# Kernel tuning notes

Measured on AMD Instinct MI355X. Metric: run time of the kernel, lower is better.

The kernel has to match this reference:

```python
import jax, jax.numpy as jnp
import numpy as np

F_IN = 22 * 1000   # flattened EEG trial
D_DENSE = 100      # Dense(100) -> becomes T=100 timesteps of dim 1
H = 128            # LSTM units
N_CLASS = 4


def setup_inputs() -> dict:
    key = jax.random.key(0)
    ks = jax.random.split(key, 8)
    B = 4096
    s1 = 1.0 / np.sqrt(F_IN)
    sr = 1.0 / np.sqrt(H)
    x = jax.random.normal(ks[0], (B, 22, 1000), dtype=jnp.float32)
    W1 = jax.random.uniform(ks[1], (F_IN, D_DENSE), jnp.float32, -s1, s1)
    b1 = jnp.zeros((D_DENSE,), jnp.float32)
    # Keras LSTM kernels: input kernel [1, 4H], recurrent kernel [H, 4H], bias [4H]
    Wk = jax.random.uniform(ks[2], (1, 4 * H), jnp.float32, -1.0, 1.0)
    Wr = jax.random.normal(ks[3], (H, 4 * H), dtype=jnp.float32) * sr
    # Keras unit_forget_bias: f-gate bias initialized to 1
    bl = jnp.concatenate([jnp.zeros(H), jnp.ones(H), jnp.zeros(2 * H)]).astype(jnp.float32)
    W2 = jax.random.uniform(ks[4], (H, N_CLASS), jnp.float32, -sr, sr)
    b2 = jnp.zeros((N_CLASS,), jnp.float32)
    return {"x": x, "W1": W1, "b1": b1, "Wk": Wk, "Wr": Wr, "bl": bl, "W2": W2, "b2": b2}


def _lstm_last(seq, Wk, Wr, bl):
    # seq: [B, T, 1]; returns final hidden state [B, H]
    B = seq.shape[0]
    # precompute input contribution for all steps: [T, B, 4H]
    zx = jnp.einsum('btf,fg->tbg', seq, Wk) + bl

    def step(carry, zxt):
        h, c = carry
        z = zxt + h @ Wr                      # [B, 4H]
        i, f, g, o = jnp.split(z, 4, axis=-1)  # keras gate order: i, f, c, o
        i = jax.nn.sigmoid(i)
        f = jax.nn.sigmoid(f)
        g = jnp.tanh(g)
        o = jax.nn.sigmoid(o)
        c = f * c + i * g
        h = o * jnp.tanh(c)
        return (h, c), None

    init = (jnp.zeros((B, H), seq.dtype), jnp.zeros((B, H), seq.dtype))
    (h, _), _ = jax.lax.scan(step, init, zx)
    return h


def reference(x, W1, b1, Wk, Wr, bl, W2, b2):
    B = x.shape[0]
    flat = x.reshape(B, -1)                 # Flatten
    d = flat @ W1 + b1                      # Dense(100), linear activation
    seq = d.reshape(B, D_DENSE, 1)          # Reshape((100, 1))
    h = _lstm_last(seq, Wk, Wr, bl)         # LSTM(128) -> last hidden state
    logits = h @ W2 + b2                    # Dense(4)
    return jax.nn.softmax(logits, axis=-1)
```

## Files before the change

kernel.cpp:

```cpp
#include <hip/hip_runtime.h>
#include <stdint.h>

#define F_IN   22000
#define B_SZ   4096
#define T_STEPS 100
#define NSPLIT 16
#define NCHUNK 22
#define KSPAN  (NCHUNK * 64)
#define ACC_STRIDE 104
#define ACCB_BYTES ((size_t)B_SZ * ACC_STRIDE * 4)
#define BIMG_BYTES 28672
#define BIMG_HALF  14336
#define W1IMG_BYTES ((size_t)NSPLIT * NCHUNK * BIMG_BYTES)

typedef float f32x4 __attribute__((ext_vector_type(4)));
typedef short s16x8 __attribute__((ext_vector_type(8)));

__device__ inline unsigned short f2bf(float f){
  unsigned u = __builtin_bit_cast(unsigned, f);
  u += 0x7FFFu + ((u >> 16) & 1u);
  return (unsigned short)(u >> 16);
}
__device__ inline float bf2f(unsigned short h){
  return __builtin_bit_cast(float, ((unsigned)h) << 16);
}
__device__ inline float sigf(float x){
  return __builtin_amdgcn_rcpf(1.f + __expf(-x));
}
__device__ inline float tanhf_(float x){
  return 1.f - 2.f * __builtin_amdgcn_rcpf(__expf(2.f * x) + 1.f);
}

__global__ __launch_bounds__(256) void k_zero(float4* __restrict__ p, int n4){
  int i = blockIdx.x * 256 + threadIdx.x;
  if (i < n4) p[i] = make_float4(0.f, 0.f, 0.f, 0.f);
}

__global__ __launch_bounds__(256) void k_w1img(const float* __restrict__ W1,
                                               char* __restrict__ img){
  int ch = blockIdx.x, s = blockIdx.y;
  int k0 = s * KSPAN + ch * 64;
  char* base = img + ((size_t)(s * NCHUNK + ch)) * BIMG_BYTES;
  int tid = threadIdx.x;
  #pragma unroll
  for (int it = 0; it < 4; ++it){
    int task = it * 256 + tid;
    if (task < 896){
      int p  = task * 16;
      int c  = p >> 7;
      int k8 = ((p >> 4) & 7) ^ (c & 7);
      unsigned hw[4], lw[4];
      #pragma unroll
      for (int jj = 0; jj < 4; ++jj){
        float v0 = 0.f, v1 = 0.f;
        int k = k0 + k8 * 8 + jj * 2;
        if (c < 100){
          if (k     < F_IN) v0 = W1[(size_t)k * 100 + c];
          if (k + 1 < F_IN) v1 = W1[(size_t)(k + 1) * 100 + c];
        }
        unsigned short h0 = f2bf(v0), l0 = f2bf(v0 - bf2f(h0));
        unsigned short h1 = f2bf(v1), l1 = f2bf(v1 - bf2f(h1));
        hw[jj] = (unsigned)h0 | ((unsigned)h1 << 16);
        lw[jj] = (unsigned)l0 | ((unsigned)l1 << 16);
      }
      *(uint4*)(base + p)             = make_uint4(hw[0], hw[1], hw[2], hw[3]);
      *(uint4*)(base + BIMG_HALF + p) = make_uint4(lw[0], lw[1], lw[2], lw[3]);
    }
  }
}

__global__ __launch_bounds__(256, 4) void k_dense(const float* __restrict__ x,
                                                  const float* __restrict__ W1,
                                                  const char* __restrict__ img,
                                                  float* __restrict__ accb,
                                                  int use_img){
  __shared__ char Bimg[BIMG_BYTES];
  int tid = threadIdx.x;
  int lane = tid & 63, w = tid >> 6;
  int r = lane & 15, oct = lane >> 4;
  int brow = blockIdx.x * 64;
  int s = blockIdx.y;
  int arow = brow + w * 16 + r;
  const float* xrow = x + (size_t)arow * F_IN;

  f32x4 acc[7];
  #pragma unroll
  for (int i = 0; i < 7; ++i) acc[i] = (f32x4)0.f;

  for (int ch = 0; ch < NCHUNK; ++ch){
    int k0 = s * KSPAN + ch * 64;
    int ka0 = k0 + oct * 8;
    int ka1 = k0 + 32 + oct * 8;
    float4 a0 = make_float4(0,0,0,0), a1 = a0, a2 = a0, a3 = a0;
    if (ka0 < F_IN){ a0 = *(const float4*)(xrow + ka0); a1 = *(const float4*)(xrow + ka0 + 4); }
    if (ka1 < F_IN){ a2 = *(const float4*)(xrow + ka1); a3 = *(const float4*)(xrow + ka1 + 4); }

    __syncthreads();
    if (use_img){
      const char* src = img + ((size_t)(s * NCHUNK + ch)) * BIMG_BYTES;
      #pragma unroll
      for (int i = 0; i < 7; ++i){
        int seg = i * 4 + w;
        __builtin_amdgcn_global_load_lds(
            (const __attribute__((address_space(1))) void*)(src + seg * 1024 + lane * 16),
            (__attribute__((address_space(3))) void*)(Bimg + seg * 1024), 16, 0, 0);
      }
    } else {
      #pragma unroll
      for (int it = 0; it < 4; ++it){
        int task = it * 256 + tid;
        if (task < 896){
          int p  = task * 16;
          int c  = p >> 7;
          int k8 = ((p >> 4) & 7) ^ (c & 7);
          unsigned hw[4], lw[4];
          #pragma unroll
          for (int jj = 0; jj < 4; ++jj){
            float v0 = 0.f, v1 = 0.f;
            int k = k0 + k8 * 8 + jj * 2;
            if (c < 100){
              if (k     < F_IN) v0 = W1[(size_t)k * 100 + c];
              if (k + 1 < F_IN) v1 = W1[(size_t)(k + 1) * 100 + c];
            }
            unsigned short h0 = f2bf(v0), l0 = f2bf(v0 - bf2f(h0));
            unsigned short h1 = f2bf(v1), l1 = f2bf(v1 - bf2f(h1));
            hw[jj] = (unsigned)h0 | ((unsigned)h1 << 16);
            lw[jj] = (unsigned)l0 | ((unsigned)l1 << 16);
          }
          *(uint4*)(Bimg + p)             = make_uint4(hw[0], hw[1], hw[2], hw[3]);
          *(uint4*)(Bimg + BIMG_HALF + p) = make_uint4(lw[0], lw[1], lw[2], lw[3]);
        }
      }
    }

    s16x8 ah0, al0, ah1, al1;
    {
      float va[16] = {a0.x,a0.y,a0.z,a0.w, a1.x,a1.y,a1.z,a1.w,
                      a2.x,a2.y,a2.z,a2.w, a3.x,a3.y,a3.z,a3.w};
      #pragma unroll
      for (int j = 0; j < 8; ++j){
        unsigned short h = f2bf(va[j]);
        ah0[j] = (short)h; al0[j] = (short)f2bf(va[j] - bf2f(h));
      }
      #pragma unroll
      for (int j = 0; j < 8; ++j){
        unsigned short h = f2bf(va[8 + j]);
        ah1[j] = (short)h; al1[j] = (short)f2bf(va[8 + j] - bf2f(h));
      }
    }
    __syncthreads();

    #pragma unroll
    for (int ct = 0; ct < 7; ++ct){
      int c = ct * 16 + r;
      int byte0 = ((c * 128 + (0 * 4 + oct) * 16) ^ ((c & 7) << 4));
      int byte1 = ((c * 128 + (1 * 4 + oct) * 16) ^ ((c & 7) << 4));
      s16x8 bh0 = *(s16x8*)(Bimg + byte0);
      s16x8 bl0 = *(s16x8*)(Bimg + BIMG_HALF + byte0);
      s16x8 bh1 = *(s16x8*)(Bimg + byte1);
      s16x8 bl1 = *(s16x8*)(Bimg + BIMG_HALF + byte1);
      acc[ct] = __builtin_amdgcn_mfma_f32_16x16x32_bf16(ah0, bh0, acc[ct], 0, 0, 0);
      acc[ct] = __builtin_amdgcn_mfma_f32_16x16x32_bf16(ah0, bl0, acc[ct], 0, 0, 0);
      acc[ct] = __builtin_amdgcn_mfma_f32_16x16x32_bf16(al0, bh0, acc[ct], 0, 0, 0);
      acc[ct] = __builtin_amdgcn_mfma_f32_16x16x32_bf16(ah1, bh1, acc[ct], 0, 0, 0);
      acc[ct] = __builtin_amdgcn_mfma_f32_16x16x32_bf16(ah1, bl1, acc[ct], 0, 0, 0);
      acc[ct] = __builtin_amdgcn_mfma_f32_16x16x32_bf16(al1, bh1, acc[ct], 0, 0, 0);
    }
  }

  #pragma unroll
  for (int ct = 0; ct < 7; ++ct){
    int col = ct * 16 + r;
    if (col < 100){
      #pragma unroll
      for (int reg = 0; reg < 4; ++reg){
        int orow = brow + w * 16 + oct * 4 + reg;
        atomicAdd(&accb[(size_t)orow * ACC_STRIDE + col], acc[ct][reg]);
      }
    }
  }
}

__global__ __launch_bounds__(256, 1) void k_lstm(const float* __restrict__ accb,
                                                 const float* __restrict__ b1,
                                                 const float* __restrict__ Wk,
                                                 const float* __restrict__ Wr,
                                                 const float* __restrict__ bl,
                                                 const float* __restrict__ W2,
                                                 const float* __restrict__ b2,
                                                 float* __restrict__ out){
  __shared__ unsigned short hbuf[2][16 * 128];
  __shared__ float dld[16][ACC_STRIDE];
  __shared__ float hf[16][132];
  int tid = threadIdx.x;
  int lane = tid & 63, w = tid >> 6;
  int oct = lane >> 4, lr = lane & 15;
  int brow = blockIdx.x * 16;

  for (int i = tid; i < 2048; i += 256) hbuf[0][i] = 0;
  for (int i = tid; i < 16 * T_STEPS; i += 256){
    int r = i / T_STEPS, t = i % T_STEPS;
    dld[r][t] = accb[(size_t)(brow + r) * ACC_STRIDE + t] + b1[t];
  }

  float wkv[4][2], blv[4][2];
  s16x8 bfrag[4][2][4];
  #pragma unroll
  for (int G = 0; G < 4; ++G){
    #pragma unroll
    for (int tt = 0; tt < 2; ++tt){
      int col = G * 128 + w * 32 + tt * 16 + lr;
      wkv[G][tt] = Wk[col];
      blv[G][tt] = bl[col];
      #pragma unroll
      for (int kk = 0; kk < 4; ++kk){
        s16x8 f;
        #pragma unroll
        for (int j = 0; j < 8; ++j){
          int k = kk * 32 + oct * 8 + j;
          f[j] = (short)f2bf(Wr[(size_t)k * 512 + col]);
        }
        bfrag[G][tt][kk] = f;
      }
    }
  }
  float cst[2][4];
  #pragma unroll
  for (int tt = 0; tt < 2; ++tt)
    #pragma unroll
    for (int reg = 0; reg < 4; ++reg) cst[tt][reg] = 0.f;
  __syncthreads();

  for (int t = 0; t < T_STEPS; ++t){
    int cur = t & 1;
    f32x4 acc[4][2];
    float dv[4];
    #pragma unroll
    for (int reg = 0; reg < 4; ++reg) dv[reg] = dld[oct * 4 + reg][t];
    #pragma unroll
    for (int G = 0; G < 4; ++G)
      #pragma unroll
      for (int tt = 0; tt < 2; ++tt)
        #pragma unroll
        for (int reg = 0; reg < 4; ++reg)
          acc[G][tt][reg] = dv[reg] * wkv[G][tt] + blv[G][tt];
    #pragma unroll
    for (int kk = 0; kk < 4; ++kk){
      int abyte = (lr * 256 + kk * 64 + oct * 16) ^ ((lr & 7) << 4);
      s16x8 a = *(s16x8*)((char*)hbuf[cur] + abyte);
      #pragma unroll
      for (int G = 0; G < 4; ++G)
        #pragma unroll
        for (int tt = 0; tt < 2; ++tt)
          acc[G][tt] = __builtin_amdgcn_mfma_f32_16x16x32_bf16(a, bfrag[G][tt][kk], acc[G][tt], 0, 0, 0);
    }
    #pragma unroll
    for (int tt = 0; tt < 2; ++tt){
      #pragma unroll
      for (int reg = 0; reg < 4; ++reg){
        float iv = sigf(acc[0][tt][reg]);
        float fv = sigf(acc[1][tt][reg]);
        float gv = tanhf_(acc[2][tt][reg]);
        float ov = sigf(acc[3][tt][reg]);
        float cv = fv * cst[tt][reg] + iv * gv;
        cst[tt][reg] = cv;
        float hv = ov * tanhf_(cv);
        int row = oct * 4 + reg;
        int col = w * 32 + tt * 16 + lr;
        int byte = (row * 256 + col * 2) ^ ((row & 7) << 4);
        *(unsigned short*)((char*)hbuf[cur ^ 1] + byte) = f2bf(hv);
        if (t == T_STEPS - 1) hf[row][col] = hv;
      }
    }
    __syncthreads();
  }

  if (tid < 64){
    int row = tid >> 2, cl = tid & 3;
    float a = b2[cl];
    #pragma unroll 8
    for (int j = 0; j < 128; ++j) a += hf[row][j] * W2[j * 4 + cl];
    float m = fmaxf(a, __shfl_xor(a, 1));
    m = fmaxf(m, __shfl_xor(m, 2));
    float e = __expf(a - m);
    float se = e + __shfl_xor(e, 1);
    se += __shfl_xor(se, 2);
    out[(size_t)(brow + row) * 4 + cl] = e * __builtin_amdgcn_rcpf(se);
  }
}

extern "C" void kernel_launch(void* const* d_in, const int* in_sizes, int n_in,
                              void* d_out, int out_size, void* d_ws, size_t ws_size,
                              hipStream_t stream){
  const float* x  = (const float*)d_in[0];
  const float* W1 = (const float*)d_in[1];
  const float* b1 = (const float*)d_in[2];
  const float* Wk = (const float*)d_in[3];
  const float* Wr = (const float*)d_in[4];
  const float* bl = (const float*)d_in[5];
  const float* W2 = (const float*)d_in[6];
  const float* b2 = (const float*)d_in[7];
  float* out = (float*)d_out;

  float* accb = (float*)d_ws;
  char*  img  = (char*)d_ws + ACCB_BYTES;
  const int use_img = (ws_size >= ACCB_BYTES + W1IMG_BYTES) ? 1 : 0;
  const int n4 = B_SZ * ACC_STRIDE / 4;

  k_zero<<<(n4 + 255) / 256, 256, 0, stream>>>((float4*)accb, n4);
  if (use_img)
    k_w1img<<<dim3(NCHUNK, NSPLIT), 256, 0, stream>>>(W1, img);
  k_dense<<<dim3(B_SZ / 64, NSPLIT), 256, 0, stream>>>(x, W1, img, accb, use_img);
  k_lstm<<<B_SZ / 16, 256, 0, stream>>>(accb, b1, Wk, Wr, bl, W2, b2, out);
}
```

Baseline: 262.7 us.

## Double-buffer W1 image in LDS and prefetch next x chunk in dense GEMM

The dense kernel now uses two LDS buffers for the pre-split W1 bf16 image. The next chunk's async global-to-LDS copy and x register loads are issued before the MFMA work on the current chunk, so memory latency overlaps with compute and one barrier per chunk is removed. The fallback path that built the W1 image inside the kernel is dropped, so the workspace is assumed to be large enough. Doubling LDS use and lowering launch bounds to 2 blocks per CU reduces occupancy in exchange for the overlap.

```diff
diff --git a/kernel.cpp b/kernel.cpp
--- a/kernel.cpp
+++ b/kernel.cpp
@@ -69,12 +69,10 @@
   }
 }
 
-__global__ __launch_bounds__(256, 4) void k_dense(const float* __restrict__ x,
-                                                  const float* __restrict__ W1,
+__global__ __launch_bounds__(256, 2) void k_dense(const float* __restrict__ x,
                                                   const char* __restrict__ img,
-                                                  float* __restrict__ accb,
-                                                  int use_img){
-  __shared__ char Bimg[BIMG_BYTES];
+                                                  float* __restrict__ accb){
+  __shared__ char Bb0[BIMG_BYTES], Bb1[BIMG_BYTES];
   int tid = threadIdx.x;
   int lane = tid & 63, w = tid >> 6;
   int r = lane & 15, oct = lane >> 4;
@@ -82,91 +80,94 @@
   int s = blockIdx.y;
   int arow = brow + w * 16 + r;
   const float* xrow = x + (size_t)arow * F_IN;
+  const char* isrc = img + (size_t)s * NCHUNK * BIMG_BYTES;
+  int kbase = s * KSPAN;
 
   f32x4 acc[7];
   #pragma unroll
   for (int i = 0; i < 7; ++i) acc[i] = (f32x4)0.f;
 
-  for (int ch = 0; ch < NCHUNK; ++ch){
-    int k0 = s * KSPAN + ch * 64;
-    int ka0 = k0 + oct * 8;
-    int ka1 = k0 + 32 + oct * 8;
-    float4 a0 = make_float4(0,0,0,0), a1 = a0, a2 = a0, a3 = a0;
-    if (ka0 < F_IN){ a0 = *(const float4*)(xrow + ka0); a1 = *(const float4*)(xrow + ka0 + 4); }
-    if (ka1 < F_IN){ a2 = *(const float4*)(xrow + ka1); a3 = *(const float4*)(xrow + ka1 + 4); }
-
+  float4 xa0, xa1, xa2, xa3;
+  float4 ya0, ya1, ya2, ya3;
+
+#define ALOAD(CH, A0, A1, A2, A3) do{                                        \
+    int k0_ = kbase + (CH) * 64;                                             \
+    int ka0_ = k0_ + oct * 8;                                                \
+    int ka1_ = k0_ + 32 + oct * 8;                                           \
+    A0 = make_float4(0.f,0.f,0.f,0.f); A1 = A0; A2 = A0; A3 = A0;            \
+    if (ka0_ < F_IN){ A0 = *(const float4*)(xrow + ka0_);                    \
+                      A1 = *(const float4*)(xrow + ka0_ + 4); }              \
+    if (ka1_ < F_IN){ A2 = *(const float4*)(xrow + ka1_);                    \
+                      A3 = *(const float4*)(xrow + ka1_ + 4); }              \
+  }while(0)
+
+#define STAGE(CH, BUF) do{                                                   \
+    const char* src_ = isrc + (size_t)(CH) * BIMG_BYTES;                     \
+    _Pragma("unroll")                                                        \
+    for (int i_ = 0; i_ < 7; ++i_){                                          \
+      int seg_ = i_ * 4 + w;                                                 \
+      __builtin_amdgcn_global_load_lds(                                      \
+        (const __attribute__((address_space(1))) void*)(src_ + seg_ * 1024 + lane * 16), \
+        (__attribute__((address_space(3))) void*)((BUF) + seg_ * 1024), 16, 0, 0); \
+    }                                                                        \
+  }while(0)
+
+#define CONVMFMA(BUF, A0, A1, A2, A3) do{                                    \
+    float va_[16] = {A0.x,A0.y,A0.z,A0.w, A1.x,A1.y,A1.z,A1.w,               \
+                     A2.x,A2.y,A2.z,A2.w, A3.x,A3.y,A3.z,A3.w};              \
+    s16x8 ah0_, al0_, ah1_, al1_;                                            \
+    _Pragma("unroll")                                                        \
+    for (int j_ = 0; j_ < 8; ++j_){                                          \
+      unsigned short h_ = f2bf(va_[j_]);                                     \
+      ah0_[j_] = (short)h_; al0_[j_] = (short)f2bf(va_[j_] - bf2f(h_));      \
+    }                                                                        \
+    _Pragma("unroll")                                                        \
+    for (int j_ = 0; j_ < 8; ++j_){                                          \
+      unsigned short h_ = f2bf(va_[8 + j_]);                                 \
+      ah1_[j_] = (short)h_; al1_[j_] = (short)f2bf(va_[8 + j_] - bf2f(h_));  \
+    }                                                                        \
+    _Pragma("unroll")                                                        \
+    for (int ct_ = 0; ct_ < 7; ++ct_){                                       \
+      int c_ = ct_ * 16 + r;                                                 \
+      int byte0_ = ((c_ * 128 + oct * 16) ^ ((c_ & 7) << 4));                \
+      int byte1_ = ((c_ * 128 + 64 + oct * 16) ^ ((c_ & 7) << 4));           \
+      s16x8 bh0_ = *(s16x8*)((BUF) + byte0_);                                \
+      s16x8 bl0_ = *(s16x8*)((BUF) + BIMG_HALF + byte0_);                    \
+      s16x8 bh1_ = *(s16x8*)((BUF) + byte1_);                                \
+      s16x8 bl1_ = *(s16x8*)((BUF) + BIMG_HALF + byte1_);                    \
+      acc[ct_] = __builtin_amdgcn_mfma_f32_16x16x32_bf16(ah0_, bh0_, acc[ct_], 0, 0, 0); \
+      acc[ct_] = __builtin_amdgcn_mfma_f32_16x16x32_bf16(ah0_, bl0_, acc[ct_], 0, 0, 0); \
+      acc[ct_] = __builtin_amdgcn_mfma_f32_16x16x32_bf16(al0_, bh0_, acc[ct_], 0, 0, 0); \
+      acc[ct_] = __builtin_amdgcn_mfma_f32_16x16x32_bf16(ah1_, bh1_, acc[ct_], 0, 0, 0); \
+      acc[ct_] = __builtin_amdgcn_mfma_f32_16x16x32_bf16(ah1_, bl1_, acc[ct_], 0, 0, 0); \
+      acc[ct_] = __builtin_amdgcn_mfma_f32_16x16x32_bf16(al1_, bh1_, acc[ct_], 0, 0, 0); \
+    }                                                                        \
+  }while(0)
+
+  STAGE(0, Bb0);
+  ALOAD(0, xa0, xa1, xa2, xa3);
+  __syncthreads();
+
+  for (int ch = 0; ch < NCHUNK; ch += 2){
+    if (ch + 1 < NCHUNK){
+      STAGE(ch + 1, Bb1);
+      ALOAD(ch + 1, ya0, ya1, ya2, ya3);
+    }
+    CONVMFMA(Bb0, xa0, xa1, xa2, xa3);
     __syncthreads();
-    if (use_img){
-      const char* src = img + ((size_t)(s * NCHUNK + ch)) * BIMG_BYTES;
-      #pragma unroll
-      for (int i = 0; i < 7; ++i){
-        int seg = i * 4 + w;
-        __builtin_amdgcn_global_load_lds(
-            (const __attribute__((address_space(1))) void*)(src + seg * 1024 + lane * 16),
-            (__attribute__((address_space(3))) void*)(Bimg + seg * 1024), 16, 0, 0);
-      }
-    } else {
-      #pragma unroll
-      for (int it = 0; it < 4; ++it){
-        int task = it * 256 + tid;
-        if (task < 896){
-          int p  = task * 16;
-          int c  = p >> 7;
-          int k8 = ((p >> 4) & 7) ^ (c & 7);
-          unsigned hw[4], lw[4];
-          #pragma unroll
-          for (int jj = 0; jj < 4; ++jj){
-            float v0 = 0.f, v1 = 0.f;
-            int k = k0 + k8 * 8 + jj * 2;
-            if (c < 100){
-              if (k     < F_IN) v0 = W1[(size_t)k * 100 + c];
-              if (k + 1 < F_IN) v1 = W1[(size_t)(k + 1) * 100 + c];
-            }
-            unsigned short h0 = f2bf(v0), l0 = f2bf(v0 - bf2f(h0));
-            unsigned short h1 = f2bf(v1), l1 = f2bf(v1 - bf2f(h1));
-            hw[jj] = (unsigned)h0 | ((unsigned)h1 << 16);
-            lw[jj] = (unsigned)l0 | ((unsigned)l1 << 16);
-          }
-          *(uint4*)(Bimg + p)             = make_uint4(hw[0], hw[1], hw[2], hw[3]);
-          *(uint4*)(Bimg + BIMG_HALF + p) = make_uint4(lw[0], lw[1], lw[2], lw[3]);
-        }
-      }
-    }
-
-    s16x8 ah0, al0, ah1, al1;
-    {
-      float va[16] = {a0.x,a0.y,a0.z,a0.w, a1.x,a1.y,a1.z,a1.w,
-                      a2.x,a2.y,a2.z,a2.w, a3.x,a3.y,a3.z,a3.w};
-      #pragma unroll
-      for (int j = 0; j < 8; ++j){
-        unsigned short h = f2bf(va[j]);
-        ah0[j] = (short)h; al0[j] = (short)f2bf(va[j] - bf2f(h));
-      }
-      #pragma unroll
-      for (int j = 0; j < 8; ++j){
-        unsigned short h = f2bf(va[8 + j]);
-        ah1[j] = (short)h; al1[j] = (short)f2bf(va[8 + j] - bf2f(h));
-      }
-    }
-    __syncthreads();
-
-    #pragma unroll
-    for (int ct = 0; ct < 7; ++ct){
-      int c = ct * 16 + r;
-      int byte0 = ((c * 128 + (0 * 4 + oct) * 16) ^ ((c & 7) << 4));
-      int byte1 = ((c * 128 + (1 * 4 + oct) * 16) ^ ((c & 7) << 4));
-      s16x8 bh0 = *(s16x8*)(Bimg + byte0);
-      s16x8 bl0 = *(s16x8*)(Bimg + BIMG_HALF + byte0);
-      s16x8 bh1 = *(s16x8*)(Bimg + byte1);
-      s16x8 bl1 = *(s16x8*)(Bimg + BIMG_HALF + byte1);
-      acc[ct] = __builtin_amdgcn_mfma_f32_16x16x32_bf16(ah0, bh0, acc[ct], 0, 0, 0);
-      acc[ct] = __builtin_amdgcn_mfma_f32_16x16x32_bf16(ah0, bl0, acc[ct], 0, 0, 0);
-      acc[ct] = __builtin_amdgcn_mfma_f32_16x16x32_bf16(al0, bh0, acc[ct], 0, 0, 0);
-      acc[ct] = __builtin_amdgcn_mfma_f32_16x16x32_bf16(ah1, bh1, acc[ct], 0, 0, 0);
-      acc[ct] = __builtin_amdgcn_mfma_f32_16x16x32_bf16(ah1, bl1, acc[ct], 0, 0, 0);
-      acc[ct] = __builtin_amdgcn_mfma_f32_16x16x32_bf16(al1, bh1, acc[ct], 0, 0, 0);
-    }
-  }
+    if (ch + 1 < NCHUNK){
+      if (ch + 2 < NCHUNK){
+        STAGE(ch + 2, Bb0);
+        ALOAD(ch + 2, xa0, xa1, xa2, xa3);
+      }
+      CONVMFMA(Bb1, ya0, ya1, ya2, ya3);
+      __syncthreads();
+    }
+  }
+
+#undef ALOAD
+#undef STAGE
+#undef CONVMFMA
 
   #pragma unroll
   for (int ct = 0; ct < 7; ++ct){
@@ -304,12 +305,10 @@
 
   float* accb = (float*)d_ws;
   char*  img  = (char*)d_ws + ACCB_BYTES;
-  const int use_img = (ws_size >= ACCB_BYTES + W1IMG_BYTES) ? 1 : 0;
   const int n4 = B_SZ * ACC_STRIDE / 4;
 
   k_zero<<<(n4 + 255) / 256, 256, 0, stream>>>((float4*)accb, n4);
-  if (use_img)
-    k_w1img<<<dim3(NCHUNK, NSPLIT), 256, 0, stream>>>(W1, img);
-  k_dense<<<dim3(B_SZ / 64, NSPLIT), 256, 0, stream>>>(x, W1, img, accb, use_img);
+  k_w1img<<<dim3(NCHUNK, NSPLIT), 256, 0, stream>>>(W1, img);
+  k_dense<<<dim3(B_SZ / 64, NSPLIT), 256, 0, stream>>>(x, img, accb);
   k_lstm<<<B_SZ / 16, 256, 0, stream>>>(accb, b1, Wk, Wr, bl, W2, b2, out);
 }
```

New measurement: 262.2 us. Within noise of the previous version (-0.2%).
